# Kernel tuning notes

Measured on AMD Instinct MI355X. Metric: run time of the kernel, lower is better.

## Reference

```python
import jax, jax.numpy as jnp
import numpy as np

B, S, H = 8, 1, 4096
NH, HD = 32, 128
P = 2047  # tokens already in cache


def setup_inputs() -> dict:
    key = jax.random.key(0)
    ks = jax.random.split(key, 7)
    w_scale = 1.0 / np.sqrt(H)
    return {
        "x": jax.random.normal(ks[0], (B, S, H), dtype=jnp.float32),
        "cache_k": jax.random.normal(ks[1], (P, B, NH, HD), dtype=jnp.float32),
        "cache_v": jax.random.normal(ks[2], (P, B, NH, HD), dtype=jnp.float32),
        "Wqkv": jax.random.normal(ks[3], (H, 3 * H), dtype=jnp.float32) * w_scale,
        "bqkv": jax.random.normal(ks[4], (3 * H,), dtype=jnp.float32) * 0.01,
        "Wproj": jax.random.normal(ks[5], (H, H), dtype=jnp.float32) * w_scale,
        "bproj": jax.random.normal(ks[6], (H,), dtype=jnp.float32) * 0.01,
        "cache_pos": P,
    }


def reference(x, cache_k, cache_v, Wqkv, bqkv, Wproj, bproj, cache_pos):
    b, s, h = x.shape
    qkv = x @ Wqkv + bqkv                              # [B,S,3H]
    q, k, v = jnp.split(qkv, 3, axis=-1)
    q = q.reshape(b, s, NH, HD).transpose(0, 2, 1, 3)  # [B,NH,S,HD]
    k = k.reshape(b, s, NH, HD).transpose(0, 2, 1, 3)
    v = v.reshape(b, s, NH, HD).transpose(0, 2, 1, 3)
    # NaiveKVCache.append stores only token 0's k/v at position cache_pos
    new_k = k[:, :, 0, :]                              # [B,NH,HD]
    new_v = v[:, :, 0, :]
    ck = jnp.concatenate([cache_k, new_k[None]], axis=0)  # [T,B,NH,HD], T=cache_pos+1
    cv = jnp.concatenate([cache_v, new_v[None]], axis=0)
    ck = ck.transpose(1, 2, 0, 3)                      # [B,NH,T,HD]
    cv = cv.transpose(1, 2, 0, 3)
    scale = 1.0 / jnp.sqrt(jnp.asarray(HD, dtype=x.dtype))
    scores = jnp.einsum("bhsd,bhtd->bhst", q, ck) * scale
    attn = jax.nn.softmax(scores, axis=-1)
    out = jnp.einsum("bhst,bhtd->bhsd", attn, cv)      # [B,NH,S,HD]
    out = out.transpose(0, 2, 1, 3).reshape(b, s, h)
    return out @ Wproj + bproj
```

## Files before the change

kernel.cpp:

```cpp
#include <hip/hip_runtime.h>

#define B 8
#define H 4096
#define NH 32
#define HD 128
#define P 2047
#define T 2048
#define HQKV 12288

__global__ __launch_bounds__(256) void init_bias_kernel(
    const float* __restrict__ bqkv, const float* __restrict__ bproj,
    float* __restrict__ qkv, float* __restrict__ out)
{
    int i = blockIdx.x * 256 + threadIdx.x;
    if (i < B * HQKV) {
        qkv[i] = bqkv[i % HQKV];
    } else {
        int j = i - B * HQKV;
        if (j < B * H) out[j] = bproj[j & (H - 1)];
    }
}

#define QKV_CB 12
#define QKV_KSPLIT 32
#define QKV_KCHUNK 128

__global__ __launch_bounds__(256) void qkv_gemm_kernel(
    const float* __restrict__ x, const float* __restrict__ W,
    float* __restrict__ qkv)
{
    const int cb = blockIdx.x % QKV_CB;
    const int kc = blockIdx.x / QKV_CB;
    const int c0 = cb * 1024 + threadIdx.x * 4;
    const int k0 = kc * QKV_KCHUNK;

    float4 acc[B];
#pragma unroll
    for (int b = 0; b < B; ++b) acc[b] = make_float4(0.f, 0.f, 0.f, 0.f);

    const float* wp = W + (size_t)k0 * HQKV + c0;
    const float* xp = x + k0;

    for (int k = 0; k < QKV_KCHUNK; k += 4) {
        float4 w0 = *(const float4*)(wp + (size_t)(k + 0) * HQKV);
        float4 w1 = *(const float4*)(wp + (size_t)(k + 1) * HQKV);
        float4 w2 = *(const float4*)(wp + (size_t)(k + 2) * HQKV);
        float4 w3 = *(const float4*)(wp + (size_t)(k + 3) * HQKV);
#pragma unroll
        for (int b = 0; b < B; ++b) {
            float4 xv = *(const float4*)(xp + b * H + k);
            acc[b].x += xv.x * w0.x + xv.y * w1.x + xv.z * w2.x + xv.w * w3.x;
            acc[b].y += xv.x * w0.y + xv.y * w1.y + xv.z * w2.y + xv.w * w3.y;
            acc[b].z += xv.x * w0.z + xv.y * w1.z + xv.z * w2.z + xv.w * w3.z;
            acc[b].w += xv.x * w0.w + xv.y * w1.w + xv.z * w2.w + xv.w * w3.w;
        }
    }
#pragma unroll
    for (int b = 0; b < B; ++b) {
        float* q = qkv + b * HQKV + c0;
        atomicAdd(q + 0, acc[b].x);
        atomicAdd(q + 1, acc[b].y);
        atomicAdd(q + 2, acc[b].z);
        atomicAdd(q + 3, acc[b].w);
    }
}

#define AT_NW 16

__global__ __launch_bounds__(1024) void attn_kernel(
    const float* __restrict__ cache_k, const float* __restrict__ cache_v,
    const float* __restrict__ qkv, float* __restrict__ attn_out)
{
    __shared__ float sc[T];
    __shared__ float wred[AT_NW];
    __shared__ float ored[AT_NW][HD];
    __shared__ float s_stats[2];

    const int b    = blockIdx.x >> 5;
    const int h    = blockIdx.x & 31;
    const int tid  = threadIdx.x;
    const int wave = tid >> 6;
    const int lane = tid & 63;
    const float scale = 0.08838834764831845f;

    const float* qp = qkv + b * HQKV + h * HD;
    float2 q2 = *(const float2*)(qp + 2 * lane);

    const float* kbase = cache_k + (size_t)b * NH * HD + h * HD + 2 * lane;
    const float* knew  = qkv + b * HQKV + H + h * HD + 2 * lane;

#pragma unroll 2
    for (int t = wave; t < T; t += AT_NW) {
        const float* kp = (t < P) ? (kbase + (size_t)t * (B * NH * HD)) : knew;
        float2 k2 = *(const float2*)kp;
        float ps = q2.x * k2.x + q2.y * k2.y;
#pragma unroll
        for (int off = 32; off >= 1; off >>= 1) ps += __shfl_xor(ps, off);
        if (lane == 0) sc[t] = ps * scale;
    }
    __syncthreads();

    float m = -1e30f;
    for (int i = tid; i < T; i += 1024) m = fmaxf(m, sc[i]);
#pragma unroll
    for (int off = 32; off >= 1; off >>= 1) m = fmaxf(m, __shfl_xor(m, off));
    if (lane == 0) wred[wave] = m;
    __syncthreads();
    if (tid == 0) {
        float mm = wred[0];
#pragma unroll
        for (int w = 1; w < AT_NW; ++w) mm = fmaxf(mm, wred[w]);
        s_stats[0] = mm;
    }
    __syncthreads();
    const float gm = s_stats[0];
    float ls = 0.f;
    for (int i = tid; i < T; i += 1024) {
        float p = __expf(sc[i] - gm);
        sc[i] = p;
        ls += p;
    }
#pragma unroll
    for (int off = 32; off >= 1; off >>= 1) ls += __shfl_xor(ls, off);
    if (lane == 0) wred[wave] = ls;
    __syncthreads();
    if (tid == 0) {
        float ss = 0.f;
#pragma unroll
        for (int w = 0; w < AT_NW; ++w) ss += wred[w];
        s_stats[1] = ss;
    }
    __syncthreads();
    const float inv_l = 1.0f / s_stats[1];

    const float* vbase = cache_v + (size_t)b * NH * HD + h * HD + 2 * lane;
    const float* vnew  = qkv + b * HQKV + 2 * H + h * HD + 2 * lane;
    float2 o2 = make_float2(0.f, 0.f);
#pragma unroll 2
    for (int t = wave; t < T; t += AT_NW) {
        const float* vp = (t < P) ? (vbase + (size_t)t * (B * NH * HD)) : vnew;
        float2 v2 = *(const float2*)vp;
        float p = sc[t];
        o2.x += p * v2.x;
        o2.y += p * v2.y;
    }
    *(float2*)&ored[wave][2 * lane] = o2;
    __syncthreads();
    if (tid < HD) {
        float s = 0.f;
#pragma unroll
        for (int w = 0; w < AT_NW; ++w) s += ored[w][tid];
        attn_out[b * H + h * HD + tid] = s * inv_l;
    }
}

#define PR_CB 4
#define PR_KSPLIT 64
#define PR_KCHUNK 64

__global__ __launch_bounds__(256) void proj_gemm_kernel(
    const float* __restrict__ attn, const float* __restrict__ W,
    float* __restrict__ out)
{
    const int cb = blockIdx.x % PR_CB;
    const int kc = blockIdx.x / PR_CB;
    const int c0 = cb * 1024 + threadIdx.x * 4;
    const int k0 = kc * PR_KCHUNK;

    float4 acc[B];
#pragma unroll
    for (int b = 0; b < B; ++b) acc[b] = make_float4(0.f, 0.f, 0.f, 0.f);

    const float* wp = W + (size_t)k0 * H + c0;
    const float* xp = attn + k0;

    for (int k = 0; k < PR_KCHUNK; k += 4) {
        float4 w0 = *(const float4*)(wp + (size_t)(k + 0) * H);
        float4 w1 = *(const float4*)(wp + (size_t)(k + 1) * H);
        float4 w2 = *(const float4*)(wp + (size_t)(k + 2) * H);
        float4 w3 = *(const float4*)(wp + (size_t)(k + 3) * H);
#pragma unroll
        for (int b = 0; b < B; ++b) {
            float4 xv = *(const float4*)(xp + b * H + k);
            acc[b].x += xv.x * w0.x + xv.y * w1.x + xv.z * w2.x + xv.w * w3.x;
            acc[b].y += xv.x * w0.y + xv.y * w1.y + xv.z * w2.y + xv.w * w3.y;
            acc[b].z += xv.x * w0.z + xv.y * w1.z + xv.z * w2.z + xv.w * w3.z;
            acc[b].w += xv.x * w0.w + xv.y * w1.w + xv.z * w2.w + xv.w * w3.w;
        }
    }
#pragma unroll
    for (int b = 0; b < B; ++b) {
        float* o = out + b * H + c0;
        atomicAdd(o + 0, acc[b].x);
        atomicAdd(o + 1, acc[b].y);
        atomicAdd(o + 2, acc[b].z);
        atomicAdd(o + 3, acc[b].w);
    }
}

extern "C" void kernel_launch(void* const* d_in, const int* in_sizes, int n_in,
                              void* d_out, int out_size, void* d_ws, size_t ws_size,
                              hipStream_t stream)
{
    const float* x       = (const float*)d_in[0];
    const float* cache_k = (const float*)d_in[1];
    const float* cache_v = (const float*)d_in[2];
    const float* Wqkv    = (const float*)d_in[3];
    const float* bqkv    = (const float*)d_in[4];
    const float* Wproj   = (const float*)d_in[5];
    const float* bproj   = (const float*)d_in[6];

    float* qkv      = (float*)d_ws;
    float* attn_out = qkv + B * HQKV;
    float* out      = (float*)d_out;

    hipLaunchKernelGGL(init_bias_kernel,
                       dim3((B * HQKV + B * H) / 256), dim3(256), 0, stream,
                       bqkv, bproj, qkv, out);
    hipLaunchKernelGGL(qkv_gemm_kernel,
                       dim3(QKV_CB * QKV_KSPLIT), dim3(256), 0, stream,
                       x, Wqkv, qkv);
    hipLaunchKernelGGL(attn_kernel,
                       dim3(B * NH), dim3(1024), 0, stream,
                       cache_k, cache_v, qkv, attn_out);
    hipLaunchKernelGGL(proj_gemm_kernel,
                       dim3(PR_CB * PR_KSPLIT), dim3(256), 0, stream,
                       attn_out, Wproj, out);
}
```

Before: 768.1 us.

## Fuse QKV GEMM, attention and projection into one cooperative kernel

Replaces the four separate launches (bias init, QKV GEMM, attention, projection) with a single cooperative kernel that uses grid-wide syncs between phases. Bias is added by the first K-chunk instead of a separate init pass, and attention loads use float4 with two tokens per wave iteration. This removes launch gaps and the bias kernel, but the GEMM phases now run with fewer concurrent waves per CU and pay grid-sync costs.

```diff
diff --git a/kernel.cpp b/kernel.cpp
--- a/kernel.cpp
+++ b/kernel.cpp
@@ -1,4 +1,7 @@
 #include <hip/hip_runtime.h>
+#include <hip/hip_cooperative_groups.h>
+
+namespace cg = cooperative_groups;
 
 #define B 8
 #define H 4096
@@ -8,193 +11,215 @@
 #define T 2048
 #define HQKV 12288
 
-__global__ __launch_bounds__(256) void init_bias_kernel(
-    const float* __restrict__ bqkv, const float* __restrict__ bproj,
-    float* __restrict__ qkv, float* __restrict__ out)
+__global__ __launch_bounds__(1024, 4) void fused_attn_kernel(
+    const float* __restrict__ x,
+    const float* __restrict__ cache_k,
+    const float* __restrict__ cache_v,
+    const float* __restrict__ Wqkv,
+    const float* __restrict__ bqkv,
+    const float* __restrict__ Wproj,
+    const float* __restrict__ bproj,
+    float* __restrict__ qkv,
+    float* __restrict__ attn_out,
+    float* __restrict__ out)
 {
-    int i = blockIdx.x * 256 + threadIdx.x;
-    if (i < B * HQKV) {
-        qkv[i] = bqkv[i % HQKV];
-    } else {
-        int j = i - B * HQKV;
-        if (j < B * H) out[j] = bproj[j & (H - 1)];
-    }
-}
-
-#define QKV_CB 12
-#define QKV_KSPLIT 32
-#define QKV_KCHUNK 128
-
-__global__ __launch_bounds__(256) void qkv_gemm_kernel(
-    const float* __restrict__ x, const float* __restrict__ W,
-    float* __restrict__ qkv)
-{
-    const int cb = blockIdx.x % QKV_CB;
-    const int kc = blockIdx.x / QKV_CB;
-    const int c0 = cb * 1024 + threadIdx.x * 4;
-    const int k0 = kc * QKV_KCHUNK;
-
-    float4 acc[B];
-#pragma unroll
-    for (int b = 0; b < B; ++b) acc[b] = make_float4(0.f, 0.f, 0.f, 0.f);
-
-    const float* wp = W + (size_t)k0 * HQKV + c0;
-    const float* xp = x + k0;
-
-    for (int k = 0; k < QKV_KCHUNK; k += 4) {
-        float4 w0 = *(const float4*)(wp + (size_t)(k + 0) * HQKV);
-        float4 w1 = *(const float4*)(wp + (size_t)(k + 1) * HQKV);
-        float4 w2 = *(const float4*)(wp + (size_t)(k + 2) * HQKV);
-        float4 w3 = *(const float4*)(wp + (size_t)(k + 3) * HQKV);
-#pragma unroll
-        for (int b = 0; b < B; ++b) {
-            float4 xv = *(const float4*)(xp + b * H + k);
-            acc[b].x += xv.x * w0.x + xv.y * w1.x + xv.z * w2.x + xv.w * w3.x;
-            acc[b].y += xv.x * w0.y + xv.y * w1.y + xv.z * w2.y + xv.w * w3.y;
-            acc[b].z += xv.x * w0.z + xv.y * w1.z + xv.z * w2.z + xv.w * w3.z;
-            acc[b].w += xv.x * w0.w + xv.y * w1.w + xv.z * w2.w + xv.w * w3.w;
-        }
-    }
-#pragma unroll
-    for (int b = 0; b < B; ++b) {
-        float* q = qkv + b * HQKV + c0;
-        atomicAdd(q + 0, acc[b].x);
-        atomicAdd(q + 1, acc[b].y);
-        atomicAdd(q + 2, acc[b].z);
-        atomicAdd(q + 3, acc[b].w);
-    }
-}
-
-#define AT_NW 16
-
-__global__ __launch_bounds__(1024) void attn_kernel(
-    const float* __restrict__ cache_k, const float* __restrict__ cache_v,
-    const float* __restrict__ qkv, float* __restrict__ attn_out)
-{
-    __shared__ float sc[T];
-    __shared__ float wred[AT_NW];
-    __shared__ float ored[AT_NW][HD];
-    __shared__ float s_stats[2];
-
-    const int b    = blockIdx.x >> 5;
-    const int h    = blockIdx.x & 31;
+    cg::grid_group grid = cg::this_grid();
+
     const int tid  = threadIdx.x;
     const int wave = tid >> 6;
     const int lane = tid & 63;
-    const float scale = 0.08838834764831845f;
-
-    const float* qp = qkv + b * HQKV + h * HD;
-    float2 q2 = *(const float2*)(qp + 2 * lane);
-
-    const float* kbase = cache_k + (size_t)b * NH * HD + h * HD + 2 * lane;
-    const float* knew  = qkv + b * HQKV + H + h * HD + 2 * lane;
-
-#pragma unroll 2
-    for (int t = wave; t < T; t += AT_NW) {
-        const float* kp = (t < P) ? (kbase + (size_t)t * (B * NH * HD)) : knew;
-        float2 k2 = *(const float2*)kp;
-        float ps = q2.x * k2.x + q2.y * k2.y;
-#pragma unroll
-        for (int off = 32; off >= 1; off >>= 1) ps += __shfl_xor(ps, off);
-        if (lane == 0) sc[t] = ps * scale;
-    }
-    __syncthreads();
-
-    float m = -1e30f;
-    for (int i = tid; i < T; i += 1024) m = fmaxf(m, sc[i]);
-#pragma unroll
-    for (int off = 32; off >= 1; off >>= 1) m = fmaxf(m, __shfl_xor(m, off));
-    if (lane == 0) wred[wave] = m;
-    __syncthreads();
-    if (tid == 0) {
-        float mm = wred[0];
-#pragma unroll
-        for (int w = 1; w < AT_NW; ++w) mm = fmaxf(mm, wred[w]);
-        s_stats[0] = mm;
-    }
-    __syncthreads();
-    const float gm = s_stats[0];
-    float ls = 0.f;
-    for (int i = tid; i < T; i += 1024) {
-        float p = __expf(sc[i] - gm);
-        sc[i] = p;
-        ls += p;
-    }
-#pragma unroll
-    for (int off = 32; off >= 1; off >>= 1) ls += __shfl_xor(ls, off);
-    if (lane == 0) wred[wave] = ls;
-    __syncthreads();
-    if (tid == 0) {
-        float ss = 0.f;
-#pragma unroll
-        for (int w = 0; w < AT_NW; ++w) ss += wred[w];
-        s_stats[1] = ss;
-    }
-    __syncthreads();
-    const float inv_l = 1.0f / s_stats[1];
-
-    const float* vbase = cache_v + (size_t)b * NH * HD + h * HD + 2 * lane;
-    const float* vnew  = qkv + b * HQKV + 2 * H + h * HD + 2 * lane;
-    float2 o2 = make_float2(0.f, 0.f);
-#pragma unroll 2
-    for (int t = wave; t < T; t += AT_NW) {
-        const float* vp = (t < P) ? (vbase + (size_t)t * (B * NH * HD)) : vnew;
-        float2 v2 = *(const float2*)vp;
-        float p = sc[t];
-        o2.x += p * v2.x;
-        o2.y += p * v2.y;
-    }
-    *(float2*)&ored[wave][2 * lane] = o2;
-    __syncthreads();
-    if (tid < HD) {
-        float s = 0.f;
-#pragma unroll
-        for (int w = 0; w < AT_NW; ++w) s += ored[w][tid];
-        attn_out[b * H + h * HD + tid] = s * inv_l;
-    }
-}
-
-#define PR_CB 4
-#define PR_KSPLIT 64
-#define PR_KCHUNK 64
-
-__global__ __launch_bounds__(256) void proj_gemm_kernel(
-    const float* __restrict__ attn, const float* __restrict__ W,
-    float* __restrict__ out)
-{
-    const int cb = blockIdx.x % PR_CB;
-    const int kc = blockIdx.x / PR_CB;
-    const int c0 = cb * 1024 + threadIdx.x * 4;
-    const int k0 = kc * PR_KCHUNK;
-
-    float4 acc[B];
-#pragma unroll
-    for (int b = 0; b < B; ++b) acc[b] = make_float4(0.f, 0.f, 0.f, 0.f);
-
-    const float* wp = W + (size_t)k0 * H + c0;
-    const float* xp = attn + k0;
-
-    for (int k = 0; k < PR_KCHUNK; k += 4) {
-        float4 w0 = *(const float4*)(wp + (size_t)(k + 0) * H);
-        float4 w1 = *(const float4*)(wp + (size_t)(k + 1) * H);
-        float4 w2 = *(const float4*)(wp + (size_t)(k + 2) * H);
-        float4 w3 = *(const float4*)(wp + (size_t)(k + 3) * H);
+
+    {
+        int g = blockIdx.x * 1024 + tid;
+        float4 z = make_float4(0.f, 0.f, 0.f, 0.f);
+        if (g < 24576) {
+            ((float4*)qkv)[g] = z;
+        } else if (g < 32768) {
+            ((float4*)out)[g - 24576] = z;
+        }
+    }
+    grid.sync();
+
+    if (wave < 6) {
+        const int id  = blockIdx.x * 6 + wave;
+        const int kc  = id / 48;
+        const int cgq = id % 48;
+        const int col = cgq * 256 + lane * 4;
+        const int k0  = kc * 128;
+
+        float4 acc[B];
+#pragma unroll
+        for (int b = 0; b < B; ++b) acc[b] = make_float4(0.f, 0.f, 0.f, 0.f);
+
+        const float* wp = Wqkv + (size_t)k0 * HQKV + col;
+        const float* xp = x + k0;
+
+        for (int k = 0; k < 128; k += 4) {
+            float4 w0 = *(const float4*)(wp + (size_t)(k + 0) * HQKV);
+            float4 w1 = *(const float4*)(wp + (size_t)(k + 1) * HQKV);
+            float4 w2 = *(const float4*)(wp + (size_t)(k + 2) * HQKV);
+            float4 w3 = *(const float4*)(wp + (size_t)(k + 3) * HQKV);
+#pragma unroll
+            for (int b = 0; b < B; ++b) {
+                float4 xv = *(const float4*)(xp + b * H + k);
+                acc[b].x += xv.x * w0.x + xv.y * w1.x + xv.z * w2.x + xv.w * w3.x;
+                acc[b].y += xv.x * w0.y + xv.y * w1.y + xv.z * w2.y + xv.w * w3.y;
+                acc[b].z += xv.x * w0.z + xv.y * w1.z + xv.z * w2.z + xv.w * w3.z;
+                acc[b].w += xv.x * w0.w + xv.y * w1.w + xv.z * w2.w + xv.w * w3.w;
+            }
+        }
+        if (kc == 0) {
+            float4 bias = *(const float4*)(bqkv + col);
+#pragma unroll
+            for (int b = 0; b < B; ++b) {
+                acc[b].x += bias.x; acc[b].y += bias.y;
+                acc[b].z += bias.z; acc[b].w += bias.w;
+            }
+        }
 #pragma unroll
         for (int b = 0; b < B; ++b) {
-            float4 xv = *(const float4*)(xp + b * H + k);
-            acc[b].x += xv.x * w0.x + xv.y * w1.x + xv.z * w2.x + xv.w * w3.x;
-            acc[b].y += xv.x * w0.y + xv.y * w1.y + xv.z * w2.y + xv.w * w3.y;
-            acc[b].z += xv.x * w0.z + xv.y * w1.z + xv.z * w2.z + xv.w * w3.z;
-            acc[b].w += xv.x * w0.w + xv.y * w1.w + xv.z * w2.w + xv.w * w3.w;
-        }
-    }
-#pragma unroll
-    for (int b = 0; b < B; ++b) {
-        float* o = out + b * H + c0;
-        atomicAdd(o + 0, acc[b].x);
-        atomicAdd(o + 1, acc[b].y);
-        atomicAdd(o + 2, acc[b].z);
-        atomicAdd(o + 3, acc[b].w);
+            float* q = qkv + b * HQKV + col;
+            atomicAdd(q + 0, acc[b].x);
+            atomicAdd(q + 1, acc[b].y);
+            atomicAdd(q + 2, acc[b].z);
+            atomicAdd(q + 3, acc[b].w);
+        }
+    }
+    grid.sync();
+
+    __shared__ float sc[T];
+    __shared__ float wred[16];
+    __shared__ float ored[16][HD];
+    __shared__ float s_stats[2];
+
+    {
+        const int b    = blockIdx.x >> 5;
+        const int h    = blockIdx.x & 31;
+        const int sl   = lane & 31;
+        const int half = lane >> 5;
+        const float scale = 0.08838834764831845f;
+        const size_t tstride = (size_t)B * NH * HD;
+
+        const float* qp = qkv + b * HQKV + h * HD;
+        float4 q4 = *(const float4*)(qp + 4 * sl);
+
+        const float* kbase = cache_k + ((size_t)b * NH + h) * HD + 4 * sl;
+        const float* knew  = qkv + b * HQKV + H + h * HD + 4 * sl;
+
+#pragma unroll 4
+        for (int pr = wave; pr < T / 2; pr += 16) {
+            int t = 2 * pr + half;
+            const float* kp = (t < P) ? (kbase + (size_t)t * tstride) : knew;
+            float4 k4 = *(const float4*)kp;
+            float ps = q4.x * k4.x + q4.y * k4.y + q4.z * k4.z + q4.w * k4.w;
+#pragma unroll
+            for (int off = 16; off >= 1; off >>= 1) ps += __shfl_xor(ps, off);
+            if (sl == 0) sc[t] = ps * scale;
+        }
+        __syncthreads();
+
+        float m = fmaxf(sc[tid], sc[tid + 1024]);
+#pragma unroll
+        for (int off = 32; off >= 1; off >>= 1) m = fmaxf(m, __shfl_xor(m, off));
+        if (lane == 0) wred[wave] = m;
+        __syncthreads();
+        if (tid == 0) {
+            float mm = wred[0];
+#pragma unroll
+            for (int w = 1; w < 16; ++w) mm = fmaxf(mm, wred[w]);
+            s_stats[0] = mm;
+        }
+        __syncthreads();
+        const float gm = s_stats[0];
+        float p0 = __expf(sc[tid] - gm);
+        float p1 = __expf(sc[tid + 1024] - gm);
+        sc[tid] = p0;
+        sc[tid + 1024] = p1;
+        float ls = p0 + p1;
+#pragma unroll
+        for (int off = 32; off >= 1; off >>= 1) ls += __shfl_xor(ls, off);
+        if (lane == 0) wred[wave] = ls;
+        __syncthreads();
+        if (tid == 0) {
+            float ss = 0.f;
+#pragma unroll
+            for (int w = 0; w < 16; ++w) ss += wred[w];
+            s_stats[1] = ss;
+        }
+        __syncthreads();
+        const float inv_l = 1.0f / s_stats[1];
+
+        const float* vbase = cache_v + ((size_t)b * NH + h) * HD + 4 * sl;
+        const float* vnew  = qkv + b * HQKV + 2 * H + h * HD + 4 * sl;
+        float4 o4 = make_float4(0.f, 0.f, 0.f, 0.f);
+#pragma unroll 4
+        for (int pr = wave; pr < T / 2; pr += 16) {
+            int t = 2 * pr + half;
+            const float* vp = (t < P) ? (vbase + (size_t)t * tstride) : vnew;
+            float4 v4 = *(const float4*)vp;
+            float p = sc[t];
+            o4.x += p * v4.x; o4.y += p * v4.y;
+            o4.z += p * v4.z; o4.w += p * v4.w;
+        }
+        o4.x += __shfl_xor(o4.x, 32);
+        o4.y += __shfl_xor(o4.y, 32);
+        o4.z += __shfl_xor(o4.z, 32);
+        o4.w += __shfl_xor(o4.w, 32);
+        if (half == 0) *(float4*)&ored[wave][4 * sl] = o4;
+        __syncthreads();
+        if (tid < HD) {
+            float s = 0.f;
+#pragma unroll
+            for (int w = 0; w < 16; ++w) s += ored[w][tid];
+            attn_out[b * H + h * HD + tid] = s * inv_l;
+        }
+    }
+    grid.sync();
+
+    if (wave < 4) {
+        const int id  = blockIdx.x * 4 + wave;
+        const int kc  = id >> 4;
+        const int cgp = id & 15;
+        const int col = cgp * 256 + lane * 4;
+        const int k0  = kc * 64;
+
+        float4 acc[B];
+#pragma unroll
+        for (int b = 0; b < B; ++b) acc[b] = make_float4(0.f, 0.f, 0.f, 0.f);
+
+        const float* wp = Wproj + (size_t)k0 * H + col;
+        const float* xp = attn_out + k0;
+
+        for (int k = 0; k < 64; k += 4) {
+            float4 w0 = *(const float4*)(wp + (size_t)(k + 0) * H);
+            float4 w1 = *(const float4*)(wp + (size_t)(k + 1) * H);
+            float4 w2 = *(const float4*)(wp + (size_t)(k + 2) * H);
+            float4 w3 = *(const float4*)(wp + (size_t)(k + 3) * H);
+#pragma unroll
+            for (int b = 0; b < B; ++b) {
+                float4 xv = *(const float4*)(xp + b * H + k);
+                acc[b].x += xv.x * w0.x + xv.y * w1.x + xv.z * w2.x + xv.w * w3.x;
+                acc[b].y += xv.x * w0.y + xv.y * w1.y + xv.z * w2.y + xv.w * w3.y;
+                acc[b].z += xv.x * w0.z + xv.y * w1.z + xv.z * w2.z + xv.w * w3.z;
+                acc[b].w += xv.x * w0.w + xv.y * w1.w + xv.z * w2.w + xv.w * w3.w;
+            }
+        }
+        if (kc == 0) {
+            float4 bias = *(const float4*)(bproj + col);
+#pragma unroll
+            for (int b = 0; b < B; ++b) {
+                acc[b].x += bias.x; acc[b].y += bias.y;
+                acc[b].z += bias.z; acc[b].w += bias.w;
+            }
+        }
+#pragma unroll
+        for (int b = 0; b < B; ++b) {
+            float* o = out + b * H + col;
+            atomicAdd(o + 0, acc[b].x);
+            atomicAdd(o + 1, acc[b].y);
+            atomicAdd(o + 2, acc[b].z);
+            atomicAdd(o + 3, acc[b].w);
+        }
     }
 }
 
@@ -214,16 +239,10 @@
     float* attn_out = qkv + B * HQKV;
     float* out      = (float*)d_out;
 
-    hipLaunchKernelGGL(init_bias_kernel,
-                       dim3((B * HQKV + B * H) / 256), dim3(256), 0, stream,
-                       bqkv, bproj, qkv, out);
-    hipLaunchKernelGGL(qkv_gemm_kernel,
-                       dim3(QKV_CB * QKV_KSPLIT), dim3(256), 0, stream,
-                       x, Wqkv, qkv);
-    hipLaunchKernelGGL(attn_kernel,
-                       dim3(B * NH), dim3(1024), 0, stream,
-                       cache_k, cache_v, qkv, attn_out);
-    hipLaunchKernelGGL(proj_gemm_kernel,
-                       dim3(PR_CB * PR_KSPLIT), dim3(256), 0, stream,
-                       attn_out, Wproj, out);
+    void* args[] = { (void*)&x, (void*)&cache_k, (void*)&cache_v,
+                     (void*)&Wqkv, (void*)&bqkv, (void*)&Wproj, (void*)&bproj,
+                     (void*)&qkv, (void*)&attn_out, (void*)&out };
+
+    hipLaunchCooperativeKernel((void*)fused_attn_kernel,
+                               dim3(B * NH), dim3(1024), args, 0, stream);
 }
```

After: 813.5 us. +5.9%, slower.

## Split attention over sequence chunks with a combine pass, widen GEMM unroll

Applied to the files above, without the earlier changes.

Attention becomes a split-KV scheme. 256 (b,h) pairs are each split into 8 chunks of 256 tokens, and each chunk computes a partial max, sum and output. A separate combine kernel then rescales and merges the partials. Each half-wave now loads float4 slices of K/V rows, so a 64-lane wave covers two tokens per load, and each wave issues eight independent loads at a time. The aim is more blocks in flight and more memory-level parallelism on the bandwidth-bound cache scan. The QKV and projection GEMMs unroll K by 8, and the bias init is vectorised to float4. The cost is an extra kernel launch and a small round-trip of partial results through the workspace.

```diff
diff --git a/kernel.cpp b/kernel.cpp
--- a/kernel.cpp
+++ b/kernel.cpp
@@ -8,31 +8,31 @@
 #define T 2048
 #define HQKV 12288
 
+#define TS 8
+#define TC 256
+#define AW 4
+
 __global__ __launch_bounds__(256) void init_bias_kernel(
     const float* __restrict__ bqkv, const float* __restrict__ bproj,
     float* __restrict__ qkv, float* __restrict__ out)
 {
     int i = blockIdx.x * 256 + threadIdx.x;
-    if (i < B * HQKV) {
-        qkv[i] = bqkv[i % HQKV];
+    if (i < 24576) {
+        ((float4*)qkv)[i] = ((const float4*)bqkv)[i % (HQKV / 4)];
     } else {
-        int j = i - B * HQKV;
-        if (j < B * H) out[j] = bproj[j & (H - 1)];
-    }
-}
-
-#define QKV_CB 12
-#define QKV_KSPLIT 32
-#define QKV_KCHUNK 128
+        int j = i - 24576;
+        ((float4*)out)[j] = ((const float4*)bproj)[j & (H / 4 - 1)];
+    }
+}
 
 __global__ __launch_bounds__(256) void qkv_gemm_kernel(
     const float* __restrict__ x, const float* __restrict__ W,
     float* __restrict__ qkv)
 {
-    const int cb = blockIdx.x % QKV_CB;
-    const int kc = blockIdx.x / QKV_CB;
+    const int cb = blockIdx.x % 12;
+    const int kc = blockIdx.x / 12;
     const int c0 = cb * 1024 + threadIdx.x * 4;
-    const int k0 = kc * QKV_KCHUNK;
+    const int k0 = kc * 128;
 
     float4 acc[B];
 #pragma unroll
@@ -41,18 +41,23 @@
     const float* wp = W + (size_t)k0 * HQKV + c0;
     const float* xp = x + k0;
 
-    for (int k = 0; k < QKV_KCHUNK; k += 4) {
-        float4 w0 = *(const float4*)(wp + (size_t)(k + 0) * HQKV);
-        float4 w1 = *(const float4*)(wp + (size_t)(k + 1) * HQKV);
-        float4 w2 = *(const float4*)(wp + (size_t)(k + 2) * HQKV);
-        float4 w3 = *(const float4*)(wp + (size_t)(k + 3) * HQKV);
+    for (int k = 0; k < 128; k += 8) {
+        float4 wr[8];
+#pragma unroll
+        for (int r = 0; r < 8; ++r)
+            wr[r] = *(const float4*)(wp + (size_t)(k + r) * HQKV);
 #pragma unroll
         for (int b = 0; b < B; ++b) {
-            float4 xv = *(const float4*)(xp + b * H + k);
-            acc[b].x += xv.x * w0.x + xv.y * w1.x + xv.z * w2.x + xv.w * w3.x;
-            acc[b].y += xv.x * w0.y + xv.y * w1.y + xv.z * w2.y + xv.w * w3.y;
-            acc[b].z += xv.x * w0.z + xv.y * w1.z + xv.z * w2.z + xv.w * w3.z;
-            acc[b].w += xv.x * w0.w + xv.y * w1.w + xv.z * w2.w + xv.w * w3.w;
+            float4 x0 = *(const float4*)(xp + b * H + k);
+            float4 x1 = *(const float4*)(xp + b * H + k + 4);
+            acc[b].x += x0.x*wr[0].x + x0.y*wr[1].x + x0.z*wr[2].x + x0.w*wr[3].x
+                      + x1.x*wr[4].x + x1.y*wr[5].x + x1.z*wr[6].x + x1.w*wr[7].x;
+            acc[b].y += x0.x*wr[0].y + x0.y*wr[1].y + x0.z*wr[2].y + x0.w*wr[3].y
+                      + x1.x*wr[4].y + x1.y*wr[5].y + x1.z*wr[6].y + x1.w*wr[7].y;
+            acc[b].z += x0.x*wr[0].z + x0.y*wr[1].z + x0.z*wr[2].z + x0.w*wr[3].z
+                      + x1.x*wr[4].z + x1.y*wr[5].z + x1.z*wr[6].z + x1.w*wr[7].z;
+            acc[b].w += x0.x*wr[0].w + x0.y*wr[1].w + x0.z*wr[2].w + x0.w*wr[3].w
+                      + x1.x*wr[4].w + x1.y*wr[5].w + x1.z*wr[6].w + x1.w*wr[7].w;
         }
     }
 #pragma unroll
@@ -65,107 +70,138 @@
     }
 }
 
-#define AT_NW 16
-
-__global__ __launch_bounds__(1024) void attn_kernel(
+__global__ __launch_bounds__(256) void attn_partial_kernel(
     const float* __restrict__ cache_k, const float* __restrict__ cache_v,
-    const float* __restrict__ qkv, float* __restrict__ attn_out)
-{
-    __shared__ float sc[T];
-    __shared__ float wred[AT_NW];
-    __shared__ float ored[AT_NW][HD];
-    __shared__ float s_stats[2];
-
-    const int b    = blockIdx.x >> 5;
-    const int h    = blockIdx.x & 31;
+    const float* __restrict__ qkv,
+    float* __restrict__ part_O, float* __restrict__ part_ml)
+{
+    __shared__ float sc[TC];
+    __shared__ float red[AW];
+    __shared__ float ored[AW][HD];
+    __shared__ float stats[2];
+
+    const int bh = blockIdx.x / TS;
+    const int ts = blockIdx.x % TS;
+    const int b  = bh >> 5;
+    const int h  = bh & 31;
     const int tid  = threadIdx.x;
-    const int wave = tid >> 6;
+    const int w    = tid >> 6;
     const int lane = tid & 63;
+    const int sl   = lane & 31;
+    const int half = lane >> 5;
+    const size_t tstride = (size_t)B * NH * HD;
     const float scale = 0.08838834764831845f;
-
-    const float* qp = qkv + b * HQKV + h * HD;
-    float2 q2 = *(const float2*)(qp + 2 * lane);
-
-    const float* kbase = cache_k + (size_t)b * NH * HD + h * HD + 2 * lane;
-    const float* knew  = qkv + b * HQKV + H + h * HD + 2 * lane;
-
-#pragma unroll 2
-    for (int t = wave; t < T; t += AT_NW) {
-        const float* kp = (t < P) ? (kbase + (size_t)t * (B * NH * HD)) : knew;
-        float2 k2 = *(const float2*)kp;
-        float ps = q2.x * k2.x + q2.y * k2.y;
-#pragma unroll
-        for (int off = 32; off >= 1; off >>= 1) ps += __shfl_xor(ps, off);
-        if (lane == 0) sc[t] = ps * scale;
-    }
-    __syncthreads();
-
-    float m = -1e30f;
-    for (int i = tid; i < T; i += 1024) m = fmaxf(m, sc[i]);
+    const int t0 = ts * TC;
+
+    float4 q4 = *(const float4*)(qkv + b * HQKV + h * HD + 4 * sl);
+    const float* kb = cache_k + ((size_t)b * NH + h) * HD + 4 * sl;
+    const float* kn = qkv + b * HQKV + H + h * HD + 4 * sl;
+
+    for (int i = 0; i < TC / 64; ++i) {
+        const int lp0 = i * 32 + w * 8;
+        float4 kk[8];
+#pragma unroll
+        for (int j = 0; j < 8; ++j) {
+            int t = t0 + 2 * (lp0 + j) + half;
+            const float* kp = (t < P) ? (kb + (size_t)t * tstride) : kn;
+            kk[j] = *(const float4*)kp;
+        }
+#pragma unroll
+        for (int j = 0; j < 8; ++j) {
+            float ps = q4.x*kk[j].x + q4.y*kk[j].y + q4.z*kk[j].z + q4.w*kk[j].w;
+#pragma unroll
+            for (int off = 16; off >= 1; off >>= 1) ps += __shfl_xor(ps, off);
+            if (sl == 0) sc[2 * (lp0 + j) + half] = ps * scale;
+        }
+    }
+    __syncthreads();
+
+    float m = sc[tid];
 #pragma unroll
     for (int off = 32; off >= 1; off >>= 1) m = fmaxf(m, __shfl_xor(m, off));
-    if (lane == 0) wred[wave] = m;
-    __syncthreads();
+    if (lane == 0) red[w] = m;
+    __syncthreads();
+    if (tid == 0)
+        stats[0] = fmaxf(fmaxf(red[0], red[1]), fmaxf(red[2], red[3]));
+    __syncthreads();
+    const float lm = stats[0];
+    float p = __expf(sc[tid] - lm);
+    sc[tid] = p;
+    float ls = p;
+#pragma unroll
+    for (int off = 32; off >= 1; off >>= 1) ls += __shfl_xor(ls, off);
+    if (lane == 0) red[w] = ls;
+    __syncthreads();
+    if (tid == 0) stats[1] = red[0] + red[1] + red[2] + red[3];
+
+    const float* vb = cache_v + ((size_t)b * NH + h) * HD + 4 * sl;
+    const float* vn = qkv + b * HQKV + 2 * H + h * HD + 4 * sl;
+    float4 o4 = make_float4(0.f, 0.f, 0.f, 0.f);
+    for (int i = 0; i < TC / 64; ++i) {
+        const int lp0 = i * 32 + w * 8;
+        float4 vv[8];
+#pragma unroll
+        for (int j = 0; j < 8; ++j) {
+            int t = t0 + 2 * (lp0 + j) + half;
+            const float* vp = (t < P) ? (vb + (size_t)t * tstride) : vn;
+            vv[j] = *(const float4*)vp;
+        }
+#pragma unroll
+        for (int j = 0; j < 8; ++j) {
+            float pw = sc[2 * (lp0 + j) + half];
+            o4.x += pw * vv[j].x; o4.y += pw * vv[j].y;
+            o4.z += pw * vv[j].z; o4.w += pw * vv[j].w;
+        }
+    }
+    o4.x += __shfl_xor(o4.x, 32);
+    o4.y += __shfl_xor(o4.y, 32);
+    o4.z += __shfl_xor(o4.z, 32);
+    o4.w += __shfl_xor(o4.w, 32);
+    if (half == 0) *(float4*)&ored[w][4 * sl] = o4;
+    __syncthreads();
+    if (tid < HD) {
+        float s = ored[0][tid] + ored[1][tid] + ored[2][tid] + ored[3][tid];
+        part_O[((size_t)bh * TS + ts) * HD + tid] = s;
+    }
     if (tid == 0) {
-        float mm = wred[0];
-#pragma unroll
-        for (int w = 1; w < AT_NW; ++w) mm = fmaxf(mm, wred[w]);
-        s_stats[0] = mm;
-    }
-    __syncthreads();
-    const float gm = s_stats[0];
-    float ls = 0.f;
-    for (int i = tid; i < T; i += 1024) {
-        float p = __expf(sc[i] - gm);
-        sc[i] = p;
-        ls += p;
-    }
-#pragma unroll
-    for (int off = 32; off >= 1; off >>= 1) ls += __shfl_xor(ls, off);
-    if (lane == 0) wred[wave] = ls;
-    __syncthreads();
-    if (tid == 0) {
-        float ss = 0.f;
-#pragma unroll
-        for (int w = 0; w < AT_NW; ++w) ss += wred[w];
-        s_stats[1] = ss;
-    }
-    __syncthreads();
-    const float inv_l = 1.0f / s_stats[1];
-
-    const float* vbase = cache_v + (size_t)b * NH * HD + h * HD + 2 * lane;
-    const float* vnew  = qkv + b * HQKV + 2 * H + h * HD + 2 * lane;
-    float2 o2 = make_float2(0.f, 0.f);
-#pragma unroll 2
-    for (int t = wave; t < T; t += AT_NW) {
-        const float* vp = (t < P) ? (vbase + (size_t)t * (B * NH * HD)) : vnew;
-        float2 v2 = *(const float2*)vp;
-        float p = sc[t];
-        o2.x += p * v2.x;
-        o2.y += p * v2.y;
-    }
-    *(float2*)&ored[wave][2 * lane] = o2;
-    __syncthreads();
-    if (tid < HD) {
-        float s = 0.f;
-#pragma unroll
-        for (int w = 0; w < AT_NW; ++w) s += ored[w][tid];
-        attn_out[b * H + h * HD + tid] = s * inv_l;
-    }
-}
-
-#define PR_CB 4
-#define PR_KSPLIT 64
-#define PR_KCHUNK 64
+        part_ml[(bh * TS + ts) * 2 + 0] = stats[0];
+        part_ml[(bh * TS + ts) * 2 + 1] = stats[1];
+    }
+}
+
+__global__ __launch_bounds__(128) void attn_combine_kernel(
+    const float* __restrict__ part_O, const float* __restrict__ part_ml,
+    float* __restrict__ attn_out)
+{
+    const int bh = blockIdx.x;
+    const int d  = threadIdx.x;
+
+    float mvals[TS], lvals[TS];
+    float gm = -1e30f;
+#pragma unroll
+    for (int s = 0; s < TS; ++s) {
+        mvals[s] = part_ml[(bh * TS + s) * 2 + 0];
+        lvals[s] = part_ml[(bh * TS + s) * 2 + 1];
+        gm = fmaxf(gm, mvals[s]);
+    }
+    float gl = 0.f, o = 0.f;
+#pragma unroll
+    for (int s = 0; s < TS; ++s) {
+        float f = __expf(mvals[s] - gm);
+        gl += f * lvals[s];
+        o  += f * part_O[((size_t)bh * TS + s) * HD + d];
+    }
+    attn_out[bh * HD + d] = o / gl;
+}
 
 __global__ __launch_bounds__(256) void proj_gemm_kernel(
     const float* __restrict__ attn, const float* __restrict__ W,
     float* __restrict__ out)
 {
-    const int cb = blockIdx.x % PR_CB;
-    const int kc = blockIdx.x / PR_CB;
+    const int cb = blockIdx.x % 4;
+    const int kc = blockIdx.x / 4;
     const int c0 = cb * 1024 + threadIdx.x * 4;
-    const int k0 = kc * PR_KCHUNK;
+    const int k0 = kc * 64;
 
     float4 acc[B];
 #pragma unroll
@@ -174,18 +210,23 @@
     const float* wp = W + (size_t)k0 * H + c0;
     const float* xp = attn + k0;
 
-    for (int k = 0; k < PR_KCHUNK; k += 4) {
-        float4 w0 = *(const float4*)(wp + (size_t)(k + 0) * H);
-        float4 w1 = *(const float4*)(wp + (size_t)(k + 1) * H);
-        float4 w2 = *(const float4*)(wp + (size_t)(k + 2) * H);
-        float4 w3 = *(const float4*)(wp + (size_t)(k + 3) * H);
+    for (int k = 0; k < 64; k += 8) {
+        float4 wr[8];
+#pragma unroll
+        for (int r = 0; r < 8; ++r)
+            wr[r] = *(const float4*)(wp + (size_t)(k + r) * H);
 #pragma unroll
         for (int b = 0; b < B; ++b) {
-            float4 xv = *(const float4*)(xp + b * H + k);
-            acc[b].x += xv.x * w0.x + xv.y * w1.x + xv.z * w2.x + xv.w * w3.x;
-            acc[b].y += xv.x * w0.y + xv.y * w1.y + xv.z * w2.y + xv.w * w3.y;
-            acc[b].z += xv.x * w0.z + xv.y * w1.z + xv.z * w2.z + xv.w * w3.z;
-            acc[b].w += xv.x * w0.w + xv.y * w1.w + xv.z * w2.w + xv.w * w3.w;
+            float4 x0 = *(const float4*)(xp + b * H + k);
+            float4 x1 = *(const float4*)(xp + b * H + k + 4);
+            acc[b].x += x0.x*wr[0].x + x0.y*wr[1].x + x0.z*wr[2].x + x0.w*wr[3].x
+                      + x1.x*wr[4].x + x1.y*wr[5].x + x1.z*wr[6].x + x1.w*wr[7].x;
+            acc[b].y += x0.x*wr[0].y + x0.y*wr[1].y + x0.z*wr[2].y + x0.w*wr[3].y
+                      + x1.x*wr[4].y + x1.y*wr[5].y + x1.z*wr[6].y + x1.w*wr[7].y;
+            acc[b].z += x0.x*wr[0].z + x0.y*wr[1].z + x0.z*wr[2].z + x0.w*wr[3].z
+                      + x1.x*wr[4].z + x1.y*wr[5].z + x1.z*wr[6].z + x1.w*wr[7].z;
+            acc[b].w += x0.x*wr[0].w + x0.y*wr[1].w + x0.z*wr[2].w + x0.w*wr[3].w
+                      + x1.x*wr[4].w + x1.y*wr[5].w + x1.z*wr[6].w + x1.w*wr[7].w;
         }
     }
 #pragma unroll
@@ -212,18 +253,18 @@
 
     float* qkv      = (float*)d_ws;
     float* attn_out = qkv + B * HQKV;
+    float* part_O   = attn_out + B * H;
+    float* part_ml  = part_O + 256 * TS * HD;
     float* out      = (float*)d_out;
 
-    hipLaunchKernelGGL(init_bias_kernel,
-                       dim3((B * HQKV + B * H) / 256), dim3(256), 0, stream,
+    hipLaunchKernelGGL(init_bias_kernel, dim3(128), dim3(256), 0, stream,
                        bqkv, bproj, qkv, out);
-    hipLaunchKernelGGL(qkv_gemm_kernel,
-                       dim3(QKV_CB * QKV_KSPLIT), dim3(256), 0, stream,
+    hipLaunchKernelGGL(qkv_gemm_kernel, dim3(384), dim3(256), 0, stream,
                        x, Wqkv, qkv);
-    hipLaunchKernelGGL(attn_kernel,
-                       dim3(B * NH), dim3(1024), 0, stream,
-                       cache_k, cache_v, qkv, attn_out);
-    hipLaunchKernelGGL(proj_gemm_kernel,
-                       dim3(PR_CB * PR_KSPLIT), dim3(256), 0, stream,
+    hipLaunchKernelGGL(attn_partial_kernel, dim3(256 * TS), dim3(256), 0, stream,
+                       cache_k, cache_v, qkv, part_O, part_ml);
+    hipLaunchKernelGGL(attn_combine_kernel, dim3(256), dim3(128), 0, stream,
+                       part_O, part_ml, attn_out);
+    hipLaunchKernelGGL(proj_gemm_kernel, dim3(256), dim3(256), 0, stream,
                        attn_out, Wproj, out);
 }
```

After: 739.0 us. 1.04x faster.
